# Kernel optimization log

Measured on AMD Instinct MI355X. Metric: run time of the kernel, lower is better.

## Reference

```python
import jax, jax.numpy as jnp
import numpy as np

N_STUDENT = 100000
N_ITEM = 20000
N_EDGES = 1000000
IN_CH = 128
EDGE_DIM = 32
DEC_CH = 64


def setup_inputs() -> dict:
    key = jax.random.key(0)
    ks = jax.random.split(key, 9)
    x_student = jax.random.normal(ks[0], (N_STUDENT, IN_CH), dtype=jnp.float32)
    x_item = jax.random.normal(ks[1], (N_ITEM, IN_CH), dtype=jnp.float32)
    edge_label_index = jax.random.randint(ks[2], (2, N_EDGES), 0, N_ITEM, dtype=jnp.int64)
    edge_feat = jax.random.normal(ks[3], (N_EDGES, EDGE_DIM), dtype=jnp.float32)
    offset = jax.random.normal(ks[4], (N_ITEM, 1), dtype=jnp.float32)
    # linear: (IN_CH + EDGE_DIM) -> DEC_CH ; linear_2: IN_CH -> DEC_CH
    s1 = 1.0 / np.sqrt(IN_CH + EDGE_DIM)
    s2 = 1.0 / np.sqrt(IN_CH)
    W1 = jax.random.uniform(ks[5], (IN_CH + EDGE_DIM, DEC_CH), minval=-s1, maxval=s1, dtype=jnp.float32)
    b1 = jax.random.uniform(ks[6], (DEC_CH,), minval=-s1, maxval=s1, dtype=jnp.float32)
    W2 = jax.random.uniform(ks[7], (IN_CH, DEC_CH), minval=-s2, maxval=s2, dtype=jnp.float32)
    b2 = jax.random.uniform(ks[8], (DEC_CH,), minval=-s2, maxval=s2, dtype=jnp.float32)
    return {
        "x_student": x_student, "x_item": x_item,
        "edge_label_index": edge_label_index, "edge_feat": edge_feat,
        "offset": offset, "W1": W1, "b1": b1, "W2": W2, "b2": b2,
    }


def reference(x_student, x_item, edge_label_index, edge_feat, offset, W1, b1, W2, b2):
    # Gather edge endpoints: [E, IN_CH]
    feat_s = x_student[edge_label_index[0]]
    feat_i = x_item[edge_label_index[1]]
    # x = elu(Linear(cat([feat_s, edge_feat])))  -> [E, DEC_CH]
    x = jnp.concatenate([feat_s, edge_feat], axis=-1)
    x = jax.nn.elu(x @ W1 + b1)
    # y = softplus(Linear_2(feat_i))  -> [E, DEC_CH]
    y = jax.nn.softplus(feat_i @ W2 + b2)
    # elementwise mult + sum reduce -> [E, 1]
    out = jnp.sum(x * y, axis=-1, keepdims=True)
    # offset gather by item index, add
    out = out + offset[edge_label_index[1]]
    return out
```

## Files before the change

kernel.cpp:

```cpp
#include <hip/hip_runtime.h>
#include <math.h>

#define N_STUDENT 100000
#define N_ITEM    20000
#define N_EDGES   1000000
#define IN_CH     128
#define EDGE_DIM  32
#define DEC_CH    64

#define N_ROWS    N_ITEM


typedef __attribute__((ext_vector_type(8))) short short8;
typedef __attribute__((ext_vector_type(4))) float f32x4;

__device__ __forceinline__ short bf16_rne(float f) {
    union { float f; unsigned u; } v; v.f = f;
    unsigned r = (v.u + 0x7FFFu + ((v.u >> 16) & 1u)) >> 16;
    return (short)r;
}

__device__ __forceinline__ short8 cvt8(float4 a0, float4 a1) {
    short8 s;
    s[0] = bf16_rne(a0.x); s[1] = bf16_rne(a0.y);
    s[2] = bf16_rne(a0.z); s[3] = bf16_rne(a0.w);
    s[4] = bf16_rne(a1.x); s[5] = bf16_rne(a1.y);
    s[6] = bf16_rne(a1.z); s[7] = bf16_rne(a1.w);
    return s;
}

#define PRE_BLOCKS 313

__global__ __launch_bounds__(256) void precompute_kernel(
    const float* __restrict__ x_student, const float* __restrict__ x_item,
    const float* __restrict__ W1, const float* __restrict__ b1,
    const float* __restrict__ W2, const float* __restrict__ b2,
    float* __restrict__ s_part, float* __restrict__ y_item)
{
    const int phase = (blockIdx.x >= PRE_BLOCKS);
    const int blk   = phase ? blockIdx.x - PRE_BLOCKS : blockIdx.x;
    const float* X  = phase ? x_item : x_student;
    const float* W  = phase ? W2 : W1;
    const float* B  = phase ? b2 : b1;
    float* OUT      = phase ? y_item : s_part;

    const int lane = threadIdx.x & 63;
    const int m = lane & 15, q = lane >> 4;
    const int wib = threadIdx.x >> 6;
    const int r0w = blk * 64 + wib * 16;
    if (r0w >= N_ROWS) return;

    short8 bfr[4][4];
    #pragma unroll
    for (int ks = 0; ks < 4; ++ks)
        #pragma unroll
        for (int ct = 0; ct < 4; ++ct)
            #pragma unroll
            for (int j = 0; j < 8; ++j)
                bfr[ks][ct][j] = bf16_rne(W[(ks * 32 + q * 8 + j) * DEC_CH + ct * 16 + m]);

    float bc[4];
    #pragma unroll
    for (int ct = 0; ct < 4; ++ct) bc[ct] = B[ct * 16 + m];

    int row = r0w + m;
    row = row < N_ROWS ? row : N_ROWS - 1;
    const float* xp = X + (size_t)row * IN_CH + q * 8;

    f32x4 acc[4];
    #pragma unroll
    for (int ct = 0; ct < 4; ++ct) acc[ct] = (f32x4){bc[ct], bc[ct], bc[ct], bc[ct]};

    #pragma unroll
    for (int ks = 0; ks < 4; ++ks) {
        float4 a0 = *(const float4*)(xp + ks * 32);
        float4 a1 = *(const float4*)(xp + ks * 32 + 4);
        short8 af = cvt8(a0, a1);
        #pragma unroll
        for (int ct = 0; ct < 4; ++ct)
            acc[ct] = __builtin_amdgcn_mfma_f32_16x16x32_bf16(af, bfr[ks][ct], acc[ct], 0, 0, 0);
    }

    #pragma unroll
    for (int reg = 0; reg < 4; ++reg) {
        const int orow = r0w + q * 4 + reg;
        if (orow < N_ROWS) {
            float4 fv;
            if (phase) {
                fv.x = fmaxf(acc[0][reg], 0.f) + log1pf(__expf(-fabsf(acc[0][reg])));
                fv.y = fmaxf(acc[1][reg], 0.f) + log1pf(__expf(-fabsf(acc[1][reg])));
                fv.z = fmaxf(acc[2][reg], 0.f) + log1pf(__expf(-fabsf(acc[2][reg])));
                fv.w = fmaxf(acc[3][reg], 0.f) + log1pf(__expf(-fabsf(acc[3][reg])));
            } else {
                fv.x = acc[0][reg]; fv.y = acc[1][reg];
                fv.z = acc[2][reg]; fv.w = acc[3][reg];
            }
            *(float4*)(OUT + (size_t)orow * DEC_CH + m * 4) = fv;
        }
    }
}

__global__ __launch_bounds__(256) void edge_kernel(
    const int* __restrict__ idx, const float* __restrict__ ef,
    const float* __restrict__ W1, const float* __restrict__ offset,
    const float* __restrict__ s_part, const float* __restrict__ y_item,
    float* __restrict__ out)
{
    __shared__ int2  sIdx[256];
    __shared__ float sOff[256];

    const int lane = threadIdx.x & 63;
    const int m = lane & 15, q = lane >> 4;
    const int e0 = blockIdx.x * 256;

    {
        const int t = threadIdx.x;
        if (e0 + t < N_EDGES) {
            const int is = idx[e0 + t];
            const int ii = idx[N_EDGES + e0 + t];
            sIdx[t] = make_int2(is, ii);
            sOff[t] = offset[ii];
        }
    }

    const float* Wb = W1 + IN_CH * DEC_CH;
    short8 bfr[4];
    #pragma unroll
    for (int ct = 0; ct < 4; ++ct)
        #pragma unroll
        for (int j = 0; j < 8; ++j)
            bfr[ct][j] = bf16_rne(Wb[(q * 8 + j) * DEC_CH + ct * 16 + m]);

    __syncthreads();

    const int wib = threadIdx.x >> 6;
    const int ew0 = e0 + wib * 64;
    if (ew0 >= N_EDGES) return;

    #pragma unroll
    for (int rt = 0; rt < 4; ++rt) {
        const float* ap = ef + (size_t)(ew0 + rt * 16 + m) * EDGE_DIM + q * 8;
        float4 a0 = *(const float4*)ap;
        float4 a1 = *(const float4*)(ap + 4);

        int2 ip[4];
        #pragma unroll
        for (int r = 0; r < 4; ++r)
            ip[r] = sIdx[wib * 64 + rt * 16 + q * 4 + r];

        float4 sg[4], yg[4];
        #pragma unroll
        for (int r = 0; r < 4; ++r) {
            sg[r] = *(const float4*)(s_part + (size_t)ip[r].x * DEC_CH + m * 4);
            yg[r] = *(const float4*)(y_item + (size_t)ip[r].y * DEC_CH + m * 4);
        }

        short8 af = cvt8(a0, a1);
        f32x4 acc[4];
        #pragma unroll
        for (int ct = 0; ct < 4; ++ct) {
            f32x4 z = {0.f, 0.f, 0.f, 0.f};
            acc[ct] = __builtin_amdgcn_mfma_f32_16x16x32_bf16(af, bfr[ct], z, 0, 0, 0);
        }

        float pr[4];
        #pragma unroll
        for (int r = 0; r < 4; ++r) {
            float t0 = acc[0][r] + sg[r].x;
            float t1 = acc[1][r] + sg[r].y;
            float t2 = acc[2][r] + sg[r].z;
            float t3 = acc[3][r] + sg[r].w;
            float x0 = t0 > 0.f ? t0 : (__expf(t0) - 1.f);
            float x1 = t1 > 0.f ? t1 : (__expf(t1) - 1.f);
            float x2 = t2 > 0.f ? t2 : (__expf(t2) - 1.f);
            float x3 = t3 > 0.f ? t3 : (__expf(t3) - 1.f);
            float p = x0 * yg[r].x;
            p = fmaf(x1, yg[r].y, p);
            p = fmaf(x2, yg[r].z, p);
            p = fmaf(x3, yg[r].w, p);
            pr[r] = p;
        }

        #pragma unroll
        for (int s = 1; s <= 8; s <<= 1) {
            pr[0] += __shfl_xor(pr[0], s, 64);
            pr[1] += __shfl_xor(pr[1], s, 64);
            pr[2] += __shfl_xor(pr[2], s, 64);
            pr[3] += __shfl_xor(pr[3], s, 64);
        }

        float v = (m & 3) == 0 ? pr[0]
                : (m & 3) == 1 ? pr[1]
                : (m & 3) == 2 ? pr[2] : pr[3];
        if (m < 4) {
            const int el = wib * 64 + rt * 16 + q * 4 + m;
            out[e0 + el] = v + sOff[el];
        }
    }
}

extern "C" void kernel_launch(void* const* d_in, const int* in_sizes, int n_in,
                              void* d_out, int out_size, void* d_ws, size_t ws_size,
                              hipStream_t stream) {
    const float* x_student = (const float*)d_in[0];
    const float* x_item    = (const float*)d_in[1];
    const int*   eli       = (const int*)d_in[2];
    const float* edge_feat = (const float*)d_in[3];
    const float* offset    = (const float*)d_in[4];
    const float* W1        = (const float*)d_in[5];
    const float* b1        = (const float*)d_in[6];
    const float* W2        = (const float*)d_in[7];
    const float* b2        = (const float*)d_in[8];
    float* out = (float*)d_out;

    float* s_part = (float*)d_ws;
    float* y_item = s_part + (size_t)N_ROWS * DEC_CH;

    precompute_kernel<<<2 * PRE_BLOCKS, 256, 0, stream>>>(
        x_student, x_item, W1, b1, W2, b2, s_part, y_item);
    edge_kernel<<<(N_EDGES + 255) / 256, 256, 0, stream>>>(
        eli, edge_feat, W1, offset, s_part, y_item, out);
}
```

Measured before the change: 275.0 us.

## Store precomputed tables in bf16, hoist edge loads, use nontemporal streaming

The precomputed per-student and per-item projection tables are now written as bf16 instead of fp32, which halves the bytes moved by the random gathers in the edge kernel. The edge kernel also issues all edge-feature loads and table gathers for its four row tiles before any MFMA work, so more memory requests are in flight at once. Index loads, edge-feature loads and output stores are marked nontemporal to keep streaming data out of the cache. In exchange, the tables lose precision through bf16 rounding, and the hoisted loads raise register pressure.

```diff
diff --git a/kernel.cpp b/kernel.cpp
--- a/kernel.cpp
+++ b/kernel.cpp
@@ -20,13 +20,18 @@
     return (short)r;
 }
 
-__device__ __forceinline__ short8 cvt8(float4 a0, float4 a1) {
+__device__ __forceinline__ short8 cvt8(f32x4 a0, f32x4 a1) {
     short8 s;
-    s[0] = bf16_rne(a0.x); s[1] = bf16_rne(a0.y);
-    s[2] = bf16_rne(a0.z); s[3] = bf16_rne(a0.w);
-    s[4] = bf16_rne(a1.x); s[5] = bf16_rne(a1.y);
-    s[6] = bf16_rne(a1.z); s[7] = bf16_rne(a1.w);
+    s[0] = bf16_rne(a0[0]); s[1] = bf16_rne(a0[1]);
+    s[2] = bf16_rne(a0[2]); s[3] = bf16_rne(a0[3]);
+    s[4] = bf16_rne(a1[0]); s[5] = bf16_rne(a1[1]);
+    s[6] = bf16_rne(a1[2]); s[7] = bf16_rne(a1[3]);
     return s;
+}
+
+__device__ __forceinline__ float bf2f(unsigned short u) {
+    union { unsigned u; float f; } v; v.u = ((unsigned)u) << 16;
+    return v.f;
 }
 
 #define PRE_BLOCKS 313
@@ -35,14 +40,14 @@
     const float* __restrict__ x_student, const float* __restrict__ x_item,
     const float* __restrict__ W1, const float* __restrict__ b1,
     const float* __restrict__ W2, const float* __restrict__ b2,
-    float* __restrict__ s_part, float* __restrict__ y_item)
+    unsigned short* __restrict__ s_part, unsigned short* __restrict__ y_item)
 {
     const int phase = (blockIdx.x >= PRE_BLOCKS);
     const int blk   = phase ? blockIdx.x - PRE_BLOCKS : blockIdx.x;
     const float* X  = phase ? x_item : x_student;
     const float* W  = phase ? W2 : W1;
     const float* B  = phase ? b2 : b1;
-    float* OUT      = phase ? y_item : s_part;
+    unsigned short* OUT = phase ? y_item : s_part;
 
     const int lane = threadIdx.x & 63;
     const int m = lane & 15, q = lane >> 4;
@@ -73,8 +78,8 @@
 
     #pragma unroll
     for (int ks = 0; ks < 4; ++ks) {
-        float4 a0 = *(const float4*)(xp + ks * 32);
-        float4 a1 = *(const float4*)(xp + ks * 32 + 4);
+        f32x4 a0 = *(const f32x4*)(xp + ks * 32);
+        f32x4 a1 = *(const f32x4*)(xp + ks * 32 + 4);
         short8 af = cvt8(a0, a1);
         #pragma unroll
         for (int ct = 0; ct < 4; ++ct)
@@ -85,17 +90,22 @@
     for (int reg = 0; reg < 4; ++reg) {
         const int orow = r0w + q * 4 + reg;
         if (orow < N_ROWS) {
-            float4 fv;
+            float f0, f1, f2, f3;
             if (phase) {
-                fv.x = fmaxf(acc[0][reg], 0.f) + log1pf(__expf(-fabsf(acc[0][reg])));
-                fv.y = fmaxf(acc[1][reg], 0.f) + log1pf(__expf(-fabsf(acc[1][reg])));
-                fv.z = fmaxf(acc[2][reg], 0.f) + log1pf(__expf(-fabsf(acc[2][reg])));
-                fv.w = fmaxf(acc[3][reg], 0.f) + log1pf(__expf(-fabsf(acc[3][reg])));
+                f0 = fmaxf(acc[0][reg], 0.f) + log1pf(__expf(-fabsf(acc[0][reg])));
+                f1 = fmaxf(acc[1][reg], 0.f) + log1pf(__expf(-fabsf(acc[1][reg])));
+                f2 = fmaxf(acc[2][reg], 0.f) + log1pf(__expf(-fabsf(acc[2][reg])));
+                f3 = fmaxf(acc[3][reg], 0.f) + log1pf(__expf(-fabsf(acc[3][reg])));
             } else {
-                fv.x = acc[0][reg]; fv.y = acc[1][reg];
-                fv.z = acc[2][reg]; fv.w = acc[3][reg];
+                f0 = acc[0][reg]; f1 = acc[1][reg];
+                f2 = acc[2][reg]; f3 = acc[3][reg];
             }
-            *(float4*)(OUT + (size_t)orow * DEC_CH + m * 4) = fv;
+            ushort4 sv;
+            sv.x = (unsigned short)bf16_rne(f0);
+            sv.y = (unsigned short)bf16_rne(f1);
+            sv.z = (unsigned short)bf16_rne(f2);
+            sv.w = (unsigned short)bf16_rne(f3);
+            *(ushort4*)(OUT + (size_t)orow * DEC_CH + m * 4) = sv;
         }
     }
 }
@@ -103,7 +113,7 @@
 __global__ __launch_bounds__(256) void edge_kernel(
     const int* __restrict__ idx, const float* __restrict__ ef,
     const float* __restrict__ W1, const float* __restrict__ offset,
-    const float* __restrict__ s_part, const float* __restrict__ y_item,
+    const unsigned short* __restrict__ s_part, const unsigned short* __restrict__ y_item,
     float* __restrict__ out)
 {
     __shared__ int2  sIdx[256];
@@ -116,8 +126,8 @@
     {
         const int t = threadIdx.x;
         if (e0 + t < N_EDGES) {
-            const int is = idx[e0 + t];
-            const int ii = idx[N_EDGES + e0 + t];
+            const int is = __builtin_nontemporal_load(idx + e0 + t);
+            const int ii = __builtin_nontemporal_load(idx + N_EDGES + e0 + t);
             sIdx[t] = make_int2(is, ii);
             sOff[t] = offset[ii];
         }
@@ -137,47 +147,56 @@
     const int ew0 = e0 + wib * 64;
     if (ew0 >= N_EDGES) return;
 
+    f32x4 a0[4], a1[4];
     #pragma unroll
     for (int rt = 0; rt < 4; ++rt) {
         const float* ap = ef + (size_t)(ew0 + rt * 16 + m) * EDGE_DIM + q * 8;
-        float4 a0 = *(const float4*)ap;
-        float4 a1 = *(const float4*)(ap + 4);
-
+        a0[rt] = __builtin_nontemporal_load((const f32x4*)ap);
+        a1[rt] = __builtin_nontemporal_load((const f32x4*)(ap + 4));
+    }
+
+    ushort4 sg[4][4], yg[4][4];
+    #pragma unroll
+    for (int rt = 0; rt < 4; ++rt) {
         int2 ip[4];
         #pragma unroll
         for (int r = 0; r < 4; ++r)
             ip[r] = sIdx[wib * 64 + rt * 16 + q * 4 + r];
-
-        float4 sg[4], yg[4];
         #pragma unroll
         for (int r = 0; r < 4; ++r) {
-            sg[r] = *(const float4*)(s_part + (size_t)ip[r].x * DEC_CH + m * 4);
-            yg[r] = *(const float4*)(y_item + (size_t)ip[r].y * DEC_CH + m * 4);
-        }
-
-        short8 af = cvt8(a0, a1);
+            sg[rt][r] = *(const ushort4*)(s_part + (size_t)ip[r].x * DEC_CH + m * 4);
+            yg[rt][r] = *(const ushort4*)(y_item + (size_t)ip[r].y * DEC_CH + m * 4);
+        }
+    }
+
+    short8 af[4];
+    #pragma unroll
+    for (int rt = 0; rt < 4; ++rt) af[rt] = cvt8(a0[rt], a1[rt]);
+
+    #pragma unroll
+    for (int rt = 0; rt < 4; ++rt) {
         f32x4 acc[4];
         #pragma unroll
         for (int ct = 0; ct < 4; ++ct) {
             f32x4 z = {0.f, 0.f, 0.f, 0.f};
-            acc[ct] = __builtin_amdgcn_mfma_f32_16x16x32_bf16(af, bfr[ct], z, 0, 0, 0);
+            acc[ct] = __builtin_amdgcn_mfma_f32_16x16x32_bf16(af[rt], bfr[ct], z, 0, 0, 0);
         }
 
         float pr[4];
         #pragma unroll
         for (int r = 0; r < 4; ++r) {
-            float t0 = acc[0][r] + sg[r].x;
-            float t1 = acc[1][r] + sg[r].y;
-            float t2 = acc[2][r] + sg[r].z;
-            float t3 = acc[3][r] + sg[r].w;
+            float t0 = acc[0][r] + bf2f(sg[rt][r].x);
+            float t1 = acc[1][r] + bf2f(sg[rt][r].y);
+            float t2 = acc[2][r] + bf2f(sg[rt][r].z);
+            float t3 = acc[3][r] + bf2f(sg[rt][r].w);
             float x0 = t0 > 0.f ? t0 : (__expf(t0) - 1.f);
             float x1 = t1 > 0.f ? t1 : (__expf(t1) - 1.f);
             float x2 = t2 > 0.f ? t2 : (__expf(t2) - 1.f);
             float x3 = t3 > 0.f ? t3 : (__expf(t3) - 1.f);
-            float p = x0 * yg[r].x;
-            p = fmaf(x1, yg[r].y, p);
-            p = fmaf(x2, yg[r].z, p);
-            p = fmaf(x3, yg[r].w, p);
+            float p = x0 * bf2f(yg[rt][r].x);
+            p = fmaf(x1, bf2f(yg[rt][r].y), p);
+            p = fmaf(x2, bf2f(yg[rt][r].z), p);
+            p = fmaf(x3, bf2f(yg[rt][r].w), p);
             pr[r] = p;
         }
 
@@ -194,7 +213,7 @@
                 : (m & 3) == 2 ? pr[2] : pr[3];
         if (m < 4) {
             const int el = wib * 64 + rt * 16 + q * 4 + m;
-            out[e0 + el] = v + sOff[el];
+            __builtin_nontemporal_store(v + sOff[el], &out[e0 + el]);
         }
     }
 }
@@ -213,8 +232,8 @@
     const float* b2        = (const float*)d_in[8];
     float* out = (float*)d_out;
 
-    float* s_part = (float*)d_ws;
-    float* y_item = s_part + (size_t)N_ROWS * DEC_CH;
+    unsigned short* s_part = (unsigned short*)d_ws;
+    unsigned short* y_item = s_part + (size_t)N_ROWS * DEC_CH;
 
     precompute_kernel<<<2 * PRE_BLOCKS, 256, 0, stream>>>(
         x_student, x_item, W1, b1, W2, b2, s_part, y_item);
```

Result: faster. 260.4 us (-5.3%).
